# Performance work log

Measured on AMD Instinct MI355X. Metric: run time of the kernel, lower is better.

## Reference

```python
import jax, jax.numpy as jnp
import numpy as np

DECAY = 0.8
EPS = 1e-05
COMMIT_W = 0.25
N, D, K = 32768, 128, 4096


def setup_inputs() -> dict:
    key = jax.random.key(0)
    k1, k2, k3, k4 = jax.random.split(key, 4)
    x = jax.random.normal(k1, (N, D), dtype=jnp.float32)
    embed = jax.random.normal(k2, (1, K, D), dtype=jnp.float32)
    cluster_size = jax.random.uniform(k3, (1, K), dtype=jnp.float32)
    embed_avg = jax.random.normal(k4, (1, K, D), dtype=jnp.float32)
    return {"x": x, "embed": embed, "cluster_size": cluster_size, "embed_avg": embed_avg}


def reference(x, embed, cluster_size, embed_avg):
    # x: [n, d]; embed: [1, K, d] (num_codebooks = 1, squeezed as in batched_embedding)
    e = embed[0]                                   # [K, d]
    K_ = e.shape[0]
    # negative squared euclidean distance (== -cdist^2 ordering, same argmin as -cdist)
    x2 = jnp.sum(x * x, axis=-1, keepdims=True)    # [n, 1]
    e2 = jnp.sum(e * e, axis=-1)                   # [K]
    dist = -(x2 - 2.0 * (x @ e.T) + e2)            # [n, K]
    embed_ind = jnp.argmax(dist, axis=-1)          # [n] cluster assignment (argmin distance)
    # differentiable embedding lookup (one-hot @ embed == gather)
    quantize = jnp.take(e, embed_ind, axis=0)      # [n, d]
    # EMA codebook statistics (training-time buffer updates)
    ones = jnp.ones((x.shape[0],), dtype=x.dtype)
    bins = jax.ops.segment_sum(ones, embed_ind, num_segments=K_)         # [K] bincount
    embed_sum = jax.ops.segment_sum(x, embed_ind, num_segments=K_)       # [K, d] scatter-add
    cs_new = cluster_size[0] * DECAY + (1.0 - DECAY) * bins
    ea_new = embed_avg[0] * DECAY + (1.0 - DECAY) * embed_sum
    n_total = jnp.sum(cs_new)
    cluster = (cs_new + EPS) / (n_total + K_ * EPS) * n_total            # laplace smoothing
    embed_normalized = ea_new / cluster[:, None]                         # [K, d]
    # commitment loss: mse(quantize.detach(), x) * weight
    commit_loss = COMMIT_W * jnp.mean((jax.lax.stop_gradient(quantize) - x) ** 2)
    return (quantize, embed_ind, commit_loss, cs_new[None], embed_normalized[None])
```

## Files before the change

### kernel.cpp

```cpp
#include <hip/hip_runtime.h>

#define NROWS 32768
#define DIM   128
#define KCODES 4096
#define DECAYF 0.8f
#define EPSF 1e-5f
#define COMMITW 0.25f

typedef _Float16 half8 __attribute__((ext_vector_type(8)));
typedef _Float16 half2v __attribute__((ext_vector_type(2)));
typedef float float4v __attribute__((ext_vector_type(4)));

__global__ __launch_bounds__(256) void esplit_kernel(const float* __restrict__ embed,
                                                     _Float16* __restrict__ estg,
                                                     float* __restrict__ e2h) {
    int code = blockIdx.x * 4 + (threadIdx.x >> 6);
    int lane = threadIdx.x & 63;
    float2 v = ((const float2*)(embed + (size_t)code * DIM))[lane];
    float s = v.x * v.x + v.y * v.y;
    #pragma unroll
    for (int off = 32; off > 0; off >>= 1) s += __shfl_down(s, off, 64);
    if (lane == 0) e2h[code] = 0.5f * s;

    int d = lane * 2;
    int ks = d >> 5, q = (d >> 3) & 3, j = d & 7;
    _Float16 h0 = (_Float16)v.x, l0 = (_Float16)(v.x - (float)h0);
    _Float16 h1 = (_Float16)v.y, l1 = (_Float16)(v.y - (float)h1);
    int chunk = code >> 6, c6 = code & 63;
    size_t base = (size_t)chunk * 16384;
    size_t hidx = base + (size_t)(( 0 + ks * 4 + q) * 64 + c6) * 8 + j;
    size_t lidx = base + (size_t)((16 + ks * 4 + q) * 64 + c6) * 8 + j;
    *(half2v*)&estg[hidx] = (half2v){h0, h1};
    *(half2v*)&estg[lidx] = (half2v){l0, l1};
}

__global__ __launch_bounds__(1024, 4) void argmax_kernel(const float* __restrict__ x,
                                                         const _Float16* __restrict__ estg,
                                                         const float* __restrict__ e2h,
                                                         int* __restrict__ ind,
                                                         float* __restrict__ out_ind,
                                                         int* __restrict__ bins,
                                                         float* __restrict__ loss) {
    __shared__ float rv[16][32];
    __shared__ int   ri[16][32];
    __shared__ float x2s[128];

    int tid = threadIdx.x;
    int lane = tid & 63;
    int w = tid >> 6;
    int j = w & 3;
    int rh = w >> 2;
    int m15 = lane & 15;
    int q = (lane >> 4) & 3;
    int n0 = blockIdx.x * 128;

    half8 Ah[2][4], Al[2][4];
    float xsq[2];
    #pragma unroll
    for (int rt = 0; rt < 2; ++rt) {
        xsq[rt] = 0.f;
        #pragma unroll
        for (int ks = 0; ks < 4; ++ks) {
            const float* p = x + (size_t)(n0 + rh * 32 + rt * 16 + m15) * DIM + ks * 32 + q * 8;
            float4 a = *(const float4*)p;
            float4 b = *(const float4*)(p + 4);
            float f[8] = {a.x, a.y, a.z, a.w, b.x, b.y, b.z, b.w};
            half8 H, L;
            #pragma unroll
            for (int e = 0; e < 8; ++e) {
                _Float16 h = (_Float16)f[e];
                H[e] = h;
                L[e] = (_Float16)(f[e] - (float)h);
                xsq[rt] += f[e] * f[e];
            }
            Ah[rt][ks] = H;
            Al[rt][ks] = L;
        }
        xsq[rt] += __shfl_xor(xsq[rt], 16, 64);
        xsq[rt] += __shfl_xor(xsq[rt], 32, 64);
    }
    if (j == 0 && lane < 16) {
        #pragma unroll
        for (int rt = 0; rt < 2; ++rt) x2s[rh * 32 + rt * 16 + m15] = xsq[rt];
    }

    float best[2][4];
    int   bidx[2][4];
    #pragma unroll
    for (int rt = 0; rt < 2; ++rt)
        #pragma unroll
        for (int r = 0; r < 4; ++r) { best[rt][r] = -3.0e38f; bidx[rt][r] = 0; }

    const int cm = j * 16 + m15;
    const _Float16* cb = estg + (size_t)cm * 8 + (size_t)q * 512;

    half8 BhA, BlA, BhB, BlB;
    float e2cur, e2nxt;

    BhA = *(const half8*)(cb);
    BlA = *(const half8*)(cb + 8192);
    e2cur = e2h[cm];

    #pragma unroll 1
    for (int ch = 0; ch < 64; ++ch) {
        float4v acc[2];
        #pragma unroll
        for (int rt = 0; rt < 2; ++rt) acc[rt] = (float4v){-e2cur, -e2cur, -e2cur, -e2cur};

        BhB = *(const half8*)(cb + 2048);
        BlB = *(const half8*)(cb + 8192 + 2048);
        #pragma unroll
        for (int rt = 0; rt < 2; ++rt) {
            acc[rt] = __builtin_amdgcn_mfma_f32_16x16x32_f16(Ah[rt][0], BhA, acc[rt], 0, 0, 0);
            acc[rt] = __builtin_amdgcn_mfma_f32_16x16x32_f16(Al[rt][0], BhA, acc[rt], 0, 0, 0);
            acc[rt] = __builtin_amdgcn_mfma_f32_16x16x32_f16(Ah[rt][0], BlA, acc[rt], 0, 0, 0);
        }
        BhA = *(const half8*)(cb + 4096);
        BlA = *(const half8*)(cb + 8192 + 4096);
        #pragma unroll
        for (int rt = 0; rt < 2; ++rt) {
            acc[rt] = __builtin_amdgcn_mfma_f32_16x16x32_f16(Ah[rt][1], BhB, acc[rt], 0, 0, 0);
            acc[rt] = __builtin_amdgcn_mfma_f32_16x16x32_f16(Al[rt][1], BhB, acc[rt], 0, 0, 0);
            acc[rt] = __builtin_amdgcn_mfma_f32_16x16x32_f16(Ah[rt][1], BlB, acc[rt], 0, 0, 0);
        }
        BhB = *(const half8*)(cb + 6144);
        BlB = *(const half8*)(cb + 8192 + 6144);
        #pragma unroll
        for (int rt = 0; rt < 2; ++rt) {
            acc[rt] = __builtin_amdgcn_mfma_f32_16x16x32_f16(Ah[rt][2], BhA, acc[rt], 0, 0, 0);
            acc[rt] = __builtin_amdgcn_mfma_f32_16x16x32_f16(Al[rt][2], BhA, acc[rt], 0, 0, 0);
            acc[rt] = __builtin_amdgcn_mfma_f32_16x16x32_f16(Ah[rt][2], BlA, acc[rt], 0, 0, 0);
        }
        BhA = *(const half8*)(cb + 16384);
        BlA = *(const half8*)(cb + 16384 + 8192);
        e2nxt = e2h[(ch + 1) * 64 + cm];
        #pragma unroll
        for (int rt = 0; rt < 2; ++rt) {
            acc[rt] = __builtin_amdgcn_mfma_f32_16x16x32_f16(Ah[rt][3], BhB, acc[rt], 0, 0, 0);
            acc[rt] = __builtin_amdgcn_mfma_f32_16x16x32_f16(Al[rt][3], BhB, acc[rt], 0, 0, 0);
            acc[rt] = __builtin_amdgcn_mfma_f32_16x16x32_f16(Ah[rt][3], BlB, acc[rt], 0, 0, 0);
        }

        int c = ch * 64 + cm;
        #pragma unroll
        for (int rt = 0; rt < 2; ++rt)
            #pragma unroll
            for (int r = 0; r < 4; ++r) {
                float s = acc[rt][r];
                if (s > best[rt][r]) { best[rt][r] = s; bidx[rt][r] = c; }
            }
        e2cur = e2nxt;
        cb += 16384;
    }

    #pragma unroll
    for (int rt = 0; rt < 2; ++rt)
        #pragma unroll
        for (int r = 0; r < 4; ++r) {
            float bv = best[rt][r];
            int   bi = bidx[rt][r];
            #pragma unroll
            for (int m = 1; m <= 8; m <<= 1) {
                float ov = __shfl_xor(bv, m, 64);
                int   oi = __shfl_xor(bi, m, 64);
                if (ov > bv || (ov == bv && oi < bi)) { bv = ov; bi = oi; }
            }
            if (m15 == 0) {
                int rl = rt * 16 + q * 4 + r;
                rv[w][rl] = bv;
                ri[w][rl] = bi;
            }
        }
    __syncthreads();
    if (tid < 128) {
        int rh2 = tid >> 5;
        int rl  = tid & 31;
        float bv = rv[rh2 * 4][rl];
        int   bi = ri[rh2 * 4][rl];
        #pragma unroll
        for (int jj = 1; jj < 4; ++jj) {
            float ov = rv[rh2 * 4 + jj][rl];
            int   oi = ri[rh2 * 4 + jj][rl];
            if (ov > bv || (ov == bv && oi < bi)) { bv = ov; bi = oi; }
        }
        ind[n0 + tid] = bi;
        out_ind[n0 + tid] = (float)bi;
        atomicAdd(&bins[bi], 1);
        float lp = x2s[tid] - 2.0f * bv;
        #pragma unroll
        for (int off = 32; off > 0; off >>= 1) lp += __shfl_down(lp, off, 64);
        if ((tid & 63) == 0) atomicAdd(loss, lp);
    }
}

__global__ __launch_bounds__(1024) void scan_kernel(const int* __restrict__ bins,
                                                    const float* __restrict__ cluster_size,
                                                    const float* __restrict__ loss,
                                                    int* __restrict__ offsets,
                                                    int* __restrict__ cursor,
                                                    float* __restrict__ out_cs,
                                                    float* __restrict__ ntot,
                                                    float* __restrict__ out_loss) {
    __shared__ int   wtot[16];
    __shared__ float fred[16];
    int t = threadIdx.x;
    int lane = t & 63, wv = t >> 6;
    int b[4];
    float cs[4];
    float csum = 0.f;
    int s = 0;
    #pragma unroll
    for (int e = 0; e < 4; ++e) {
        b[e] = bins[t * 4 + e];
        s += b[e];
        cs[e] = cluster_size[t * 4 + e] * DECAYF + (1.0f - DECAYF) * (float)b[e];
        csum += cs[e];
    }
    int sc = s;
    #pragma unroll
    for (int off = 1; off < 64; off <<= 1) {
        int v = __shfl_up(sc, off, 64);
        if (lane >= off) sc += v;
    }
    float fc = csum;
    #pragma unroll
    for (int off = 32; off > 0; off >>= 1) fc += __shfl_down(fc, off, 64);
    if (lane == 63) wtot[wv] = sc;
    if (lane == 0) fred[wv] = fc;
    __syncthreads();
    if (t < 16) {
        int v = wtot[t];
        int scv = v;
        #pragma unroll
        for (int off = 1; off < 16; off <<= 1) {
            int u = __shfl_up(scv, off, 64);
            if (t >= off) scv += u;
        }
        wtot[t] = scv - v;
    }
    if (t == 0) {
        float tot = 0.f;
        #pragma unroll
        for (int i = 0; i < 16; ++i) tot += fred[i];
        *ntot = tot;
        *out_loss = COMMITW * (*loss) / (float)((size_t)NROWS * DIM);
    }
    __syncthreads();
    int ex = sc - s + wtot[wv];
    #pragma unroll
    for (int e = 0; e < 4; ++e) {
        offsets[t * 4 + e] = ex;
        cursor[t * 4 + e] = ex;
        out_cs[t * 4 + e] = cs[e];
        ex += b[e];
    }
}

__global__ __launch_bounds__(256) void reorder_kernel(const int* __restrict__ ind,
                                                      int* __restrict__ cursor,
                                                      int* __restrict__ rowids,
                                                      int* __restrict__ codesorted) {
    int row = blockIdx.x * 256 + threadIdx.x;
    int k = ind[row];
    int pos = atomicAdd(&cursor[k], 1);
    rowids[pos] = row;
    codesorted[pos] = k;
}

#define WROWS 16
__global__ __launch_bounds__(256) void segred_kernel(const float* __restrict__ x,
                                                     const float* __restrict__ embed,
                                                     const int* __restrict__ rowids,
                                                     const int* __restrict__ codesorted,
                                                     const int* __restrict__ offsets,
                                                     const int* __restrict__ bins,
                                                     float* __restrict__ esum,
                                                     float* __restrict__ out_q) {
    int tid = threadIdx.x;
    int lane = tid & 63;
    int wv = blockIdx.x * 4 + (tid >> 6);
    int w0 = wv * WROWS;

    int i16 = lane & (WROWS - 1);
    int rowv = rowids[w0 + i16];
    int kv   = codesorted[w0 + i16];

    float2 xv[WROWS];
    #pragma unroll
    for (int i = 0; i < WROWS; ++i) {
        int row = __shfl(rowv, i, 64);
        xv[i] = ((const float2*)(x + (size_t)row * DIM))[lane];
    }

    int curk = __shfl(kv, 0, 64);
    float2 qv = ((const float2*)(embed + (size_t)curk * DIM))[lane];
    float2 acc = {0.f, 0.f};

    #pragma unroll
    for (int i = 0; i < WROWS; ++i) {
        int row = __shfl(rowv, i, 64);
        int k   = __shfl(kv, i, 64);
        if (k != curk) {
            int sbeg = offsets[curk];
            int send = sbeg + bins[curk];
            float* ep = esum + (size_t)curk * DIM + lane * 2;
            if (sbeg >= w0 && send <= w0 + WROWS) {
                *(float2*)ep = acc;
            } else {
                atomicAdd(ep, acc.x);
                atomicAdd(ep + 1, acc.y);
            }
            curk = k;
            acc = (float2){0.f, 0.f};
            qv = ((const float2*)(embed + (size_t)curk * DIM))[lane];
        }
        acc.x += xv[i].x;
        acc.y += xv[i].y;
        ((float2*)(out_q + (size_t)row * DIM))[lane] = qv;
    }
    {
        int sbeg = offsets[curk];
        int send = sbeg + bins[curk];
        float* ep = esum + (size_t)curk * DIM + lane * 2;
        if (sbeg >= w0 && send <= w0 + WROWS) {
            *(float2*)ep = acc;
        } else {
            atomicAdd(ep, acc.x);
            atomicAdd(ep + 1, acc.y);
        }
    }
}

__global__ __launch_bounds__(256) void norm_kernel(const float* __restrict__ esum,
                                                   const float* __restrict__ embed_avg,
                                                   const float* __restrict__ out_cs,
                                                   const float* __restrict__ ntot,
                                                   float* __restrict__ out_norm) {
    int idx = blockIdx.x * 256 + threadIdx.x;
    int k = idx >> 6;
    float nt = *ntot;
    float cs = out_cs[k];
    float cluster = (cs + EPSF) / (nt + (float)KCODES * EPSF) * nt;
    float inv = 1.0f / cluster;
    float2 es = ((const float2*)esum)[idx];
    float2 ea = ((const float2*)embed_avg)[idx];
    float2 o;
    o.x = (ea.x * DECAYF + (1.0f - DECAYF) * es.x) * inv;
    o.y = (ea.y * DECAYF + (1.0f - DECAYF) * es.y) * inv;
    ((float2*)out_norm)[idx] = o;
}

extern "C" void kernel_launch(void* const* d_in, const int* in_sizes, int n_in,
                              void* d_out, int out_size, void* d_ws, size_t ws_size,
                              hipStream_t stream) {
    const float* x            = (const float*)d_in[0];
    const float* embed        = (const float*)d_in[1];
    const float* cluster_size = (const float*)d_in[2];
    const float* embed_avg    = (const float*)d_in[3];

    float* out      = (float*)d_out;
    float* out_q    = out;
    float* out_ind  = out + 4194304;
    float* out_loss = out_ind + 32768;
    float* out_cs   = out_loss + 1;
    float* out_norm = out_cs + 4096;

    char* ws = (char*)d_ws;
    _Float16* estg = (_Float16*)ws;
    float* e2h   = (float*)(ws + 2097152);
    int*   ind   = (int*)(ws + 2113536);
    int*   offsets = (int*)(ws + 2244608);
    int*   cursor  = (int*)(ws + 2260992);
    int*   rowids  = (int*)(ws + 2277376);
    int*   codesorted = (int*)(ws + 2408448);
    float* loss  = (float*)(ws + 2539520);
    float* ntot  = loss + 1;
    int*   bins  = (int*)(ws + 2539776);
    float* esum  = (float*)(ws + 2556160);

    hipMemsetAsync(ws + 2539520, 0, 256 + 16384 + 2097152, stream);

    esplit_kernel<<<KCODES / 4, 256, 0, stream>>>(embed, estg, e2h);
    argmax_kernel<<<NROWS / 128, 1024, 0, stream>>>(x, estg, e2h, ind, out_ind,
                                                    bins, loss);
    scan_kernel<<<1, 1024, 0, stream>>>(bins, cluster_size, loss, offsets, cursor,
                                        out_cs, ntot, out_loss);
    reorder_kernel<<<NROWS / 256, 256, 0, stream>>>(ind, cursor, rowids, codesorted);
    segred_kernel<<<NROWS / WROWS / 4, 256, 0, stream>>>(x, embed, rowids, codesorted,
                                                         offsets, bins, esum, out_q);
    norm_kernel<<<KCODES * DIM / 2 / 256, 256, 0, stream>>>(esum, embed_avg, out_cs,
                                                            ntot, out_norm);
}
```

Baseline: 203.0 us.

## Stage codebook chunks into LDS via async global_load_lds double buffering

New measurement: 262.4 us. 1.29x slower.

```diff
diff --git a/kernel.cpp b/kernel.cpp
--- a/kernel.cpp
+++ b/kernel.cpp
@@ -10,6 +10,12 @@
 typedef _Float16 half8 __attribute__((ext_vector_type(8)));
 typedef _Float16 half2v __attribute__((ext_vector_type(2)));
 typedef float float4v __attribute__((ext_vector_type(4)));
+
+__device__ inline void stage1k(const _Float16* gsrc, _Float16* ldsbase) {
+    __builtin_amdgcn_global_load_lds(
+        (const __attribute__((address_space(1))) void*)gsrc,
+        (__attribute__((address_space(3))) void*)ldsbase, 16, 0, 0);
+}
 
 __global__ __launch_bounds__(256) void esplit_kernel(const float* __restrict__ embed,
                                                      _Float16* __restrict__ estg,
@@ -23,13 +29,14 @@
     if (lane == 0) e2h[code] = 0.5f * s;
 
     int d = lane * 2;
-    int ks = d >> 5, q = (d >> 3) & 3, j = d & 7;
+    int ks = d >> 5, q = (d >> 3) & 3, e = d & 7;
     _Float16 h0 = (_Float16)v.x, l0 = (_Float16)(v.x - (float)h0);
     _Float16 h1 = (_Float16)v.y, l1 = (_Float16)(v.y - (float)h1);
     int chunk = code >> 6, c6 = code & 63;
+    int jj = c6 >> 4, m15c = c6 & 15;
     size_t base = (size_t)chunk * 16384;
-    size_t hidx = base + (size_t)(( 0 + ks * 4 + q) * 64 + c6) * 8 + j;
-    size_t lidx = base + (size_t)((16 + ks * 4 + q) * 64 + c6) * 8 + j;
+    size_t hidx = base + (size_t)(((0 * 4 + ks) * 4 + jj) * 64 + q * 16 + m15c) * 8 + e;
+    size_t lidx = base + (size_t)(((1 * 4 + ks) * 4 + jj) * 64 + q * 16 + m15c) * 8 + e;
     *(half2v*)&estg[hidx] = (half2v){h0, h1};
     *(half2v*)&estg[lidx] = (half2v){l0, l1};
 }
@@ -41,6 +48,7 @@
                                                          float* __restrict__ out_ind,
                                                          int* __restrict__ bins,
                                                          float* __restrict__ loss) {
+    __shared__ __align__(16) _Float16 bstg[2][16384];
     __shared__ float rv[16][32];
     __shared__ int   ri[16][32];
     __shared__ float x2s[128];
@@ -53,6 +61,12 @@
     int m15 = lane & 15;
     int q = (lane >> 4) & 3;
     int n0 = blockIdx.x * 128;
+
+    {
+        const _Float16* g0 = estg + (size_t)(w * 2) * 512 + (size_t)lane * 8;
+        stage1k(g0, &bstg[0][(w * 2) * 512]);
+        stage1k(g0 + 512, &bstg[0][(w * 2 + 1) * 512]);
+    }
 
     half8 Ah[2][4], Al[2][4];
     float xsq[2];
@@ -92,54 +106,44 @@
         for (int r = 0; r < 4; ++r) { best[rt][r] = -3.0e38f; bidx[rt][r] = 0; }
 
     const int cm = j * 16 + m15;
-    const _Float16* cb = estg + (size_t)cm * 8 + (size_t)q * 512;
-
-    half8 BhA, BlA, BhB, BlB;
-    float e2cur, e2nxt;
-
-    BhA = *(const half8*)(cb);
-    BlA = *(const half8*)(cb + 8192);
-    e2cur = e2h[cm];
-
+    float e2cur = e2h[cm];
+
+    __syncthreads();
+
+    int cur = 0;
     #pragma unroll 1
     for (int ch = 0; ch < 64; ++ch) {
+        int chn = (ch + 1 < 64) ? ch + 1 : 0;
+        {
+            const _Float16* gn = estg + (size_t)chn * 16384 + (size_t)(w * 2) * 512 + (size_t)lane * 8;
+            _Float16* db = &bstg[cur ^ 1][(w * 2) * 512];
+            stage1k(gn, db);
+            stage1k(gn + 512, db + 512);
+        }
+        float e2n = e2h[chn * 64 + cm];
+
+        const _Float16* bufc = bstg[cur];
+        half8 Bh[4], Bl[4];
+        #pragma unroll
+        for (int ks = 0; ks < 4; ++ks) {
+            Bh[ks] = ((const half8*)(bufc + (size_t)(((0 * 4 + ks) * 4 + j) * 512)))[lane];
+            Bl[ks] = ((const half8*)(bufc + (size_t)(((1 * 4 + ks) * 4 + j) * 512)))[lane];
+        }
+
         float4v acc[2];
         #pragma unroll
         for (int rt = 0; rt < 2; ++rt) acc[rt] = (float4v){-e2cur, -e2cur, -e2cur, -e2cur};
 
-        BhB = *(const half8*)(cb + 2048);
-        BlB = *(const half8*)(cb + 8192 + 2048);
-        #pragma unroll
-        for (int rt = 0; rt < 2; ++rt) {
-            acc[rt] = __builtin_amdgcn_mfma_f32_16x16x32_f16(Ah[rt][0], BhA, acc[rt], 0, 0, 0);
-            acc[rt] = __builtin_amdgcn_mfma_f32_16x16x32_f16(Al[rt][0], BhA, acc[rt], 0, 0, 0);
-            acc[rt] = __builtin_amdgcn_mfma_f32_16x16x32_f16(Ah[rt][0], BlA, acc[rt], 0, 0, 0);
-        }
-        BhA = *(const half8*)(cb + 4096);
-        BlA = *(const half8*)(cb + 8192 + 4096);
-        #pragma unroll
-        for (int rt = 0; rt < 2; ++rt) {
-            acc[rt] = __builtin_amdgcn_mfma_f32_16x16x32_f16(Ah[rt][1], BhB, acc[rt], 0, 0, 0);
-            acc[rt] = __builtin_amdgcn_mfma_f32_16x16x32_f16(Al[rt][1], BhB, acc[rt], 0, 0, 0);
-            acc[rt] = __builtin_amdgcn_mfma_f32_16x16x32_f16(Ah[rt][1], BlB, acc[rt], 0, 0, 0);
-        }
-        BhB = *(const half8*)(cb + 6144);
-        BlB = *(const half8*)(cb + 8192 + 6144);
-        #pragma unroll
-        for (int rt = 0; rt < 2; ++rt) {
-            acc[rt] = __builtin_amdgcn_mfma_f32_16x16x32_f16(Ah[rt][2], BhA, acc[rt], 0, 0, 0);
-            acc[rt] = __builtin_amdgcn_mfma_f32_16x16x32_f16(Al[rt][2], BhA, acc[rt], 0, 0, 0);
-            acc[rt] = __builtin_amdgcn_mfma_f32_16x16x32_f16(Ah[rt][2], BlA, acc[rt], 0, 0, 0);
-        }
-        BhA = *(const half8*)(cb + 16384);
-        BlA = *(const half8*)(cb + 16384 + 8192);
-        e2nxt = e2h[(ch + 1) * 64 + cm];
-        #pragma unroll
-        for (int rt = 0; rt < 2; ++rt) {
-            acc[rt] = __builtin_amdgcn_mfma_f32_16x16x32_f16(Ah[rt][3], BhB, acc[rt], 0, 0, 0);
-            acc[rt] = __builtin_amdgcn_mfma_f32_16x16x32_f16(Al[rt][3], BhB, acc[rt], 0, 0, 0);
-            acc[rt] = __builtin_amdgcn_mfma_f32_16x16x32_f16(Ah[rt][3], BlB, acc[rt], 0, 0, 0);
-        }
+        __builtin_amdgcn_s_setprio(1);
+        #pragma unroll
+        for (int ks = 0; ks < 4; ++ks)
+            #pragma unroll
+            for (int rt = 0; rt < 2; ++rt) {
+                acc[rt] = __builtin_amdgcn_mfma_f32_16x16x32_f16(Ah[rt][ks], Bh[ks], acc[rt], 0, 0, 0);
+                acc[rt] = __builtin_amdgcn_mfma_f32_16x16x32_f16(Al[rt][ks], Bh[ks], acc[rt], 0, 0, 0);
+                acc[rt] = __builtin_amdgcn_mfma_f32_16x16x32_f16(Ah[rt][ks], Bl[ks], acc[rt], 0, 0, 0);
+            }
+        __builtin_amdgcn_s_setprio(0);
 
         int c = ch * 64 + cm;
         #pragma unroll
@@ -149,8 +153,10 @@
                 float s = acc[rt][r];
                 if (s > best[rt][r]) { best[rt][r] = s; bidx[rt][r] = c; }
             }
-        e2cur = e2nxt;
-        cb += 16384;
+        e2cur = e2n;
+
+        __syncthreads();
+        cur ^= 1;
     }
 
     #pragma unroll
```
